# Optimization experiments

Measured on AMD Instinct MI355X. Metric: run time of the kernel, lower is better.

## Reference

```python
import jax, jax.numpy as jnp
import numpy as np

DEGREE = 8


def _askey_wilson_basis(x, a, b, c, d, q, degree):
    # Iterative 3-term recurrence (same math as the recursive torch version).
    # x: (batch, input_dim); a,b,c,d,q: scalars broadcast over x.
    basis = [jnp.ones_like(x)]
    if degree >= 1:
        p1 = (2 * (1 + a * b * q) * x - (a + b) * (1 + c * d * q)) / (1 + a * b * c * d * q ** 2)
        basis.append(p1)
    for n in range(2, degree + 1):
        An = (1 - a * b * q ** (n - 1)) * (1 - c * d * q ** (n - 1)) * (1 - a * b * c * d * q ** (2 * n - 2))
        An = An / ((1 - a * b * c * d * q ** (2 * n - 1)) * (1 - a * b * c * d * q ** (2 * n)))
        Cn = (1 - q ** n) * (1 - a * b * q ** (n - 1)) * (1 - c * d * q ** (n - 1)) * (1 - a * b * c * d * q ** (2 * n - 2))
        Cn = Cn / ((1 - a * b * c * d * q ** (2 * n - 2)) * (1 - a * b * c * d * q ** (2 * n - 1)))
        pn = ((2 * x - An) * basis[n - 1] - Cn * basis[n - 2]) / (1 - q ** n)
        basis.append(pn)
    return jnp.stack(basis, axis=-1)  # (batch, input_dim, degree+1)


def setup_inputs() -> dict:
    key = jax.random.key(0)
    k1, k2, k3, k4, k5, k6, k7 = jax.random.split(key, 7)
    input_dim, output_dim, degree = 1024, 1024, DEGREE
    batch = 8192
    x = jax.random.normal(k1, (batch, input_dim), dtype=jnp.float32)
    a = jax.random.normal(k2, (1,), dtype=jnp.float32)
    b = jax.random.normal(k3, (1,), dtype=jnp.float32)
    c = jax.random.normal(k4, (1,), dtype=jnp.float32)
    d = jax.random.normal(k5, (1,), dtype=jnp.float32)
    q = jax.random.normal(k6, (1,), dtype=jnp.float32)
    std = 1.0 / (input_dim * (degree + 1))
    coeffs = jax.random.normal(k7, (input_dim, output_dim, degree + 1), dtype=jnp.float32) * std
    return {"x": x, "a": a, "b": b, "c": c, "d": d, "q": q, "coeffs": coeffs}


def reference(x, a, b, c, d, q, coeffs) -> jnp.ndarray:
    a0, b0, c0, d0, q0 = a[0], b[0], c[0], d[0], q[0]
    basis = _askey_wilson_basis(x, a0, b0, c0, d0, q0, DEGREE)  # (b, i, d+1)
    y = jnp.einsum('bid,iod->bo', basis, coeffs)
    return y
```

## Files before the change

kernel.cpp:

```cpp
#include <hip/hip_runtime.h>
#include <cstdint>

typedef unsigned short u16;
typedef __bf16 bf16x8 __attribute__((ext_vector_type(8)));
typedef float f32x4 __attribute__((ext_vector_type(4)));

#define M_DIM 8192
#define N_DIM 1024
#define I_DIM 1024
#define NDEG 8
#define K_DIM (I_DIM * NDEG)
#define BM 128
#define BN 128
#define BK 64

__device__ __forceinline__ u16 f2bf(float f) {
    union { float f; uint32_t u; } v; v.f = f;
    return (u16)((v.u + 0x7FFFu + ((v.u >> 16) & 1u)) >> 16);
}

__device__ __forceinline__ void gload_lds16(const u16* g, u16* l) {
    auto lp = reinterpret_cast<__attribute__((address_space(3))) uint32_t*>(
        reinterpret_cast<uintptr_t>(l));
    __builtin_amdgcn_global_load_lds(reinterpret_cast<const uint32_t*>(g), lp, 16, 0, 0);
}

__global__ __launch_bounds__(256) void aw_transform(
    const float* __restrict__ coeffs, u16* __restrict__ Bt, float* __restrict__ bias)
{
    __shared__ float lds[32][292];
    int bi = blockIdx.x >> 5, bo = blockIdx.x & 31;
    int i0 = bi * 32, o0 = bo * 32;
    int t = threadIdx.x;

    {
        int r = t >> 3, s = t & 7;
        const float4* src = (const float4*)(coeffs + ((size_t)(i0 + r) * N_DIM + o0) * 9);
#pragma unroll
        for (int j = 0; j < 9; ++j) {
            float4 v = src[s * 9 + j];
            *(float4*)&lds[r][(s * 9 + j) * 4] = v;
        }
    }
    __syncthreads();

    {
        int c = t >> 3, s2 = t & 7;
        u16 ob[32];
#pragma unroll
        for (int rr = 0; rr < 4; ++rr)
#pragma unroll
            for (int dd = 0; dd < 8; ++dd)
                ob[rr * 8 + dd] = f2bf(lds[s2 * 4 + rr][c * 9 + 1 + dd]);
        uint4* dst = (uint4*)(Bt + (size_t)(o0 + c) * K_DIM + (size_t)i0 * 8 + s2 * 32);
        const uint4* sp = (const uint4*)ob;
#pragma unroll
        for (int u = 0; u < 4; ++u) dst[u] = sp[u];
    }

    if (t < 32) {
        float sum = 0.f;
#pragma unroll
        for (int rr = 0; rr < 32; ++rr) sum += lds[rr][t * 9];
        atomicAdd(&bias[o0 + t], sum);
    }
}

__global__ void aw_basis(const float* __restrict__ x,
                         const float* __restrict__ pa, const float* __restrict__ pb,
                         const float* __restrict__ pc, const float* __restrict__ pd,
                         const float* __restrict__ pq,
                         u16* __restrict__ A, int row0)
{
    int t  = blockIdx.x * 256 + threadIdx.x;
    int rb = t >> 7;
    int g  = t & 127;
    int i0 = g << 3;
    int b  = row0 + rb;

    float a = *pa, bb = *pb, c = *pc, d = *pd, q = *pq;
    float ab = a * bb, cd = c * d, abcd = ab * cd;

    float qp[17];
    qp[0] = 1.f;
#pragma unroll
    for (int k = 1; k <= 16; ++k) qp[k] = qp[k - 1] * q;

    float den1 = 1.f + abcd * q * q;
    float c1x = 2.f * (1.f + ab * q) / den1;
    float c1c = -(a + bb) * (1.f + cd * q) / den1;

    float An[9], Cn[9], Sn[9];
#pragma unroll
    for (int n = 2; n <= 8; ++n) {
        float t1 = 1.f - ab * qp[n - 1];
        float t2 = 1.f - cd * qp[n - 1];
        float t3 = 1.f - abcd * qp[2 * n - 2];
        float t4 = 1.f - abcd * qp[2 * n - 1];
        float t5 = 1.f - abcd * qp[2 * n];
        An[n] = (t1 * t2 * t3) / (t4 * t5);
        Cn[n] = ((1.f - qp[n]) * t1 * t2 * t3) / (t3 * t4);
        Sn[n] = 1.f / (1.f - qp[n]);
    }

    const float4* x4 = (const float4*)(x + (size_t)b * I_DIM + i0);
    float4 v0 = x4[0], v1 = x4[1];
    float xv[8] = {v0.x, v0.y, v0.z, v0.w, v1.x, v1.y, v1.z, v1.w};

    u16 ob[64];
#pragma unroll
    for (int j = 0; j < 8; ++j) {
        float xj = xv[j];
        float p1 = c1x * xj + c1c;
        ob[j * 8 + 0] = f2bf(p1);
        float pm2 = 1.f, pm1 = p1;
#pragma unroll
        for (int n = 2; n <= 8; ++n) {
            float pn = ((2.f * xj - An[n]) * pm1 - Cn[n] * pm2) * Sn[n];
            ob[j * 8 + n - 1] = f2bf(pn);
            pm2 = pm1; pm1 = pn;
        }
    }

    uint4* dst = (uint4*)(A + (size_t)rb * K_DIM + (size_t)i0 * 8);
    const uint4* s = (const uint4*)ob;
#pragma unroll
    for (int u = 0; u < 8; ++u) dst[u] = s[u];
}

__global__ __launch_bounds__(256) void aw_gemm(
    const u16* __restrict__ A,
    const u16* __restrict__ B,
    const float* __restrict__ bias,
    float* __restrict__ C,
    int row0, int rowBlocks)
{
    __shared__ u16 As[BM * BK];
    __shared__ u16 Bs[BN * BK];

    int nwg = rowBlocks * 8;
    int bid = blockIdx.x;
    int per = nwg >> 3;
    int logical = (bid & 7) * per + (bid >> 3);
    int rowBlk = logical >> 3;
    int colBlk = logical & 7;

    int lane = threadIdx.x & 63;
    int wid  = threadIdx.x >> 6;
    int wr = wid >> 1, wc = wid & 1;

    const size_t aBase = (size_t)rowBlk * BM * K_DIM;
    const size_t bBase = (size_t)colBlk * BN * K_DIM;

    f32x4 acc[4][4];
#pragma unroll
    for (int mi = 0; mi < 4; ++mi)
#pragma unroll
        for (int ni = 0; ni < 4; ++ni)
            acc[mi][ni] = (f32x4){0.f, 0.f, 0.f, 0.f};

    const int sidx = threadIdx.x;

    for (int kt = 0; kt < K_DIM / BK; ++kt) {
        const int k0 = kt * BK;
#pragma unroll
        for (int j = 0; j < 4; ++j) {
            int idx = j * 256 + sidx;
            int r = idx >> 3, sl = idx & 7;
            int col = (sl ^ (r & 7)) << 3;
            gload_lds16(A + aBase + (size_t)r * K_DIM + k0 + col, &As[idx << 3]);
        }
#pragma unroll
        for (int j = 0; j < 4; ++j) {
            int idx = j * 256 + sidx;
            int r = idx >> 3, sl = idx & 7;
            int col = (sl ^ (r & 7)) << 3;
            gload_lds16(B + bBase + (size_t)r * K_DIM + k0 + col, &Bs[idx << 3]);
        }
        __syncthreads();

#pragma unroll
        for (int ks = 0; ks < 2; ++ks) {
            bf16x8 af[4], bfr[4];
#pragma unroll
            for (int mi = 0; mi < 4; ++mi) {
                int r = wr * 64 + mi * 16 + (lane & 15);
                int s = ks * 4 + (lane >> 4);
                af[mi] = *(const bf16x8*)((const char*)As + r * 128 + ((s ^ (r & 7)) << 4));
            }
#pragma unroll
            for (int ni = 0; ni < 4; ++ni) {
                int r = wc * 64 + ni * 16 + (lane & 15);
                int s = ks * 4 + (lane >> 4);
                bfr[ni] = *(const bf16x8*)((const char*)Bs + r * 128 + ((s ^ (r & 7)) << 4));
            }
#pragma unroll
            for (int mi = 0; mi < 4; ++mi)
#pragma unroll
                for (int ni = 0; ni < 4; ++ni)
                    acc[mi][ni] = __builtin_amdgcn_mfma_f32_16x16x32_bf16(
                        af[mi], bfr[ni], acc[mi][ni], 0, 0, 0);
        }
        __syncthreads();
    }

    int gRow = row0 + rowBlk * BM + wr * 64;
    int gCol = colBlk * BN + wc * 64;
#pragma unroll
    for (int mi = 0; mi < 4; ++mi) {
#pragma unroll
        for (int ni = 0; ni < 4; ++ni) {
            int rr = gRow + mi * 16 + ((lane >> 4) << 2);
            int cc = gCol + ni * 16 + (lane & 15);
            float bv = bias[cc];
            float* dst = C + (size_t)rr * N_DIM + cc;
#pragma unroll
            for (int j = 0; j < 4; ++j) dst[(size_t)j * N_DIM] = acc[mi][ni][j] + bv;
        }
    }
}

extern "C" void kernel_launch(void* const* d_in, const int* in_sizes, int n_in,
                              void* d_out, int out_size, void* d_ws, size_t ws_size,
                              hipStream_t stream)
{
    const float* x      = (const float*)d_in[0];
    const float* pa     = (const float*)d_in[1];
    const float* pb     = (const float*)d_in[2];
    const float* pc     = (const float*)d_in[3];
    const float* pd     = (const float*)d_in[4];
    const float* pq     = (const float*)d_in[5];
    const float* coeffs = (const float*)d_in[6];
    float* out = (float*)d_out;

    float* bias = (float*)d_ws;
    const size_t biasBytes = 4096;
    u16* Bt = (u16*)((char*)d_ws + biasBytes);
    const size_t btBytes = (size_t)N_DIM * K_DIM * sizeof(u16);
    u16* Abuf = (u16*)((char*)d_ws + biasBytes + btBytes);
    size_t used = biasBytes + btBytes;
    size_t avail = ws_size > used ? ws_size - used : 0;

    int chunk = M_DIM;
    while (chunk > 128 && (size_t)chunk * K_DIM * sizeof(u16) > avail) chunk >>= 1;

    hipMemsetAsync(bias, 0, N_DIM * sizeof(float), stream);
    aw_transform<<<1024, 256, 0, stream>>>(coeffs, Bt, bias);

    for (int row0 = 0; row0 < M_DIM; row0 += chunk) {
        aw_basis<<<(chunk * 128) / 256, 256, 0, stream>>>(x, pa, pb, pc, pd, pq, Abuf, row0);
        int rowBlocks = chunk / BM;
        aw_gemm<<<rowBlocks * 8, 256, 0, stream>>>(Abuf, Bt, bias, out, row0, rowBlocks);
    }
}
```

Measured before the change: 213.0 us.

## Triple-buffer GEMM LDS loads with 256x128 tiles and 8 waves

The GEMM now uses 512 threads per block with a 256x128 output tile, and a three-stage LDS ring buffer. Global-to-LDS loads for tile t+2 are issued before computing tile t, with explicit vmcnt waits and raw barriers replacing the load-sync-compute-sync loop. MFMA blocks are wrapped in s_setprio to favour math waves. The aim is to hide global load latency and double A-tile reuse of B, at the cost of more LDS (144KB) and lower occupancy.

Result: faster. 197.4 us (-7.3%).

```diff
diff --git a/kernel.cpp b/kernel.cpp
--- a/kernel.cpp
+++ b/kernel.cpp
@@ -10,9 +10,12 @@
 #define I_DIM 1024
 #define NDEG 8
 #define K_DIM (I_DIM * NDEG)
-#define BM 128
+#define BM 256
 #define BN 128
 #define BK 64
+#define NT (K_DIM / BK)
+#define A_TILE (BM * BK)
+#define B_TILE (BN * BK)
 
 __device__ __forceinline__ u16 f2bf(float f) {
     union { float f; uint32_t u; } v; v.f = f;
@@ -128,15 +131,15 @@
     for (int u = 0; u < 8; ++u) dst[u] = s[u];
 }
 
-__global__ __launch_bounds__(256) void aw_gemm(
+__global__ __launch_bounds__(512) void aw_gemm(
     const u16* __restrict__ A,
     const u16* __restrict__ B,
     const float* __restrict__ bias,
     float* __restrict__ C,
     int row0, int rowBlocks)
 {
-    __shared__ u16 As[BM * BK];
-    __shared__ u16 Bs[BN * BK];
+    __shared__ u16 As[3 * A_TILE];
+    __shared__ u16 Bs[3 * B_TILE];
 
     int nwg = rowBlocks * 8;
     int bid = blockIdx.x;
@@ -145,9 +148,11 @@
     int rowBlk = logical >> 3;
     int colBlk = logical & 7;
 
-    int lane = threadIdx.x & 63;
-    int wid  = threadIdx.x >> 6;
-    int wr = wid >> 1, wc = wid & 1;
+    const int tid  = threadIdx.x;
+    const int lane = tid & 63;
+    const int wid  = tid >> 6;
+    const int wr = wid & 3;
+    const int wc = wid >> 2;
 
     const size_t aBase = (size_t)rowBlk * BM * K_DIM;
     const size_t bBase = (size_t)colBlk * BN * K_DIM;
@@ -159,26 +164,29 @@
         for (int ni = 0; ni < 4; ++ni)
             acc[mi][ni] = (f32x4){0.f, 0.f, 0.f, 0.f};
 
-    const int sidx = threadIdx.x;
-
-    for (int kt = 0; kt < K_DIM / BK; ++kt) {
+    auto stage = [&](int kt, int buf) {
         const int k0 = kt * BK;
+        u16* dA = As + buf * A_TILE;
+        u16* dB = Bs + buf * B_TILE;
 #pragma unroll
         for (int j = 0; j < 4; ++j) {
-            int idx = j * 256 + sidx;
+            int idx = j * 512 + tid;
             int r = idx >> 3, sl = idx & 7;
             int col = (sl ^ (r & 7)) << 3;
-            gload_lds16(A + aBase + (size_t)r * K_DIM + k0 + col, &As[idx << 3]);
-        }
-#pragma unroll
-        for (int j = 0; j < 4; ++j) {
-            int idx = j * 256 + sidx;
+            gload_lds16(A + aBase + (size_t)r * K_DIM + k0 + col, dA + (idx << 3));
+        }
+#pragma unroll
+        for (int j = 0; j < 2; ++j) {
+            int idx = j * 512 + tid;
             int r = idx >> 3, sl = idx & 7;
             int col = (sl ^ (r & 7)) << 3;
-            gload_lds16(B + bBase + (size_t)r * K_DIM + k0 + col, &Bs[idx << 3]);
-        }
-        __syncthreads();
-
+            gload_lds16(B + bBase + (size_t)r * K_DIM + k0 + col, dB + (idx << 3));
+        }
+    };
+
+    auto compute = [&](int buf) {
+        const char* aB = (const char*)(As + buf * A_TILE);
+        const char* bB = (const char*)(Bs + buf * B_TILE);
 #pragma unroll
         for (int ks = 0; ks < 2; ++ks) {
             bf16x8 af[4], bfr[4];
@@ -186,22 +194,40 @@
             for (int mi = 0; mi < 4; ++mi) {
                 int r = wr * 64 + mi * 16 + (lane & 15);
                 int s = ks * 4 + (lane >> 4);
-                af[mi] = *(const bf16x8*)((const char*)As + r * 128 + ((s ^ (r & 7)) << 4));
+                af[mi] = *(const bf16x8*)(aB + r * 128 + ((s ^ (r & 7)) << 4));
             }
 #pragma unroll
             for (int ni = 0; ni < 4; ++ni) {
                 int r = wc * 64 + ni * 16 + (lane & 15);
                 int s = ks * 4 + (lane >> 4);
-                bfr[ni] = *(const bf16x8*)((const char*)Bs + r * 128 + ((s ^ (r & 7)) << 4));
+                bfr[ni] = *(const bf16x8*)(bB + r * 128 + ((s ^ (r & 7)) << 4));
             }
+            __builtin_amdgcn_s_setprio(1);
 #pragma unroll
             for (int mi = 0; mi < 4; ++mi)
 #pragma unroll
                 for (int ni = 0; ni < 4; ++ni)
                     acc[mi][ni] = __builtin_amdgcn_mfma_f32_16x16x32_bf16(
                         af[mi], bfr[ni], acc[mi][ni], 0, 0, 0);
-        }
-        __syncthreads();
+            __builtin_amdgcn_s_setprio(0);
+        }
+    };
+
+    stage(0, 0);
+    stage(1, 1);
+
+    for (int t = 0; t < NT; ++t) {
+        __builtin_amdgcn_s_barrier();
+        if (t + 2 < NT) {
+            stage(t + 2, (t + 2) % 3);
+            asm volatile("s_waitcnt vmcnt(12)" ::: "memory");
+        } else if (t + 1 < NT) {
+            asm volatile("s_waitcnt vmcnt(6)" ::: "memory");
+        } else {
+            asm volatile("s_waitcnt vmcnt(0)" ::: "memory");
+        }
+        __builtin_amdgcn_s_barrier();
+        compute(t % 3);
     }
 
     int gRow = row0 + rowBlk * BM + wr * 64;
@@ -242,7 +268,7 @@
     size_t avail = ws_size > used ? ws_size - used : 0;
 
     int chunk = M_DIM;
-    while (chunk > 128 && (size_t)chunk * K_DIM * sizeof(u16) > avail) chunk >>= 1;
+    while (chunk > 256 && (size_t)chunk * K_DIM * sizeof(u16) > avail) chunk >>= 1;
 
     hipMemsetAsync(bias, 0, N_DIM * sizeof(float), stream);
     aw_transform<<<1024, 256, 0, stream>>>(coeffs, Bt, bias);
@@ -250,6 +276,6 @@
     for (int row0 = 0; row0 < M_DIM; row0 += chunk) {
         aw_basis<<<(chunk * 128) / 256, 256, 0, stream>>>(x, pa, pb, pc, pd, pq, Abuf, row0);
         int rowBlocks = chunk / BM;
-        aw_gemm<<<rowBlocks * 8, 256, 0, stream>>>(Abuf, Bt, bias, out, row0, rowBlocks);
-    }
-}
+        aw_gemm<<<rowBlocks * 8, 512, 0, stream>>>(Abuf, Bt, bias, out, row0, rowBlocks);
+    }
+}
```
